# Optimization experiments

Hardware: AMD Instinct MI355X
Metric: run time of the kernel (lower is better)

Reference implementation:

```python
import jax, jax.numpy as jnp
import numpy as np

B, S, DIM = 2, 2048, 4096
NH, NKV, HD = 32, 8, 128
REP = NH // NKV
ROPE_THETA = 10000.0


def _rope(x, cos, sin):
    # x: (B, S, H, HD); cos/sin: (S, HD//2). Interleaved complex rotation.
    xr, xi = x[..., 0::2], x[..., 1::2]
    c = cos[None, :, None, :]
    s = sin[None, :, None, :]
    out_r = xr * c - xi * s
    out_i = xr * s + xi * c
    return jnp.stack([out_r, out_i], axis=-1).reshape(x.shape)


def setup_inputs() -> dict:
    key = jax.random.key(0)
    k0, k1, k2, k3, k4 = jax.random.split(key, 5)
    x = jax.random.normal(k0, (B, S, DIM), jnp.float32)
    std = 0.02
    wq = jax.random.normal(k1, (NH * HD, DIM), jnp.float32) * std
    wk = jax.random.normal(k2, (NKV * HD, DIM), jnp.float32) * std
    wv = jax.random.normal(k3, (NKV * HD, DIM), jnp.float32) * std
    wo = jax.random.normal(k4, (DIM, NH * HD), jnp.float32) * std
    inv_freq = 1.0 / (ROPE_THETA ** (jnp.arange(0, HD, 2, dtype=jnp.float32) / HD))
    ang = jnp.outer(jnp.arange(S, dtype=jnp.float32), inv_freq)  # (S, HD//2)
    return {
        "x": x, "wq": wq, "wk": wk, "wv": wv, "wo": wo,
        "freqs_cos": jnp.cos(ang), "freqs_sin": jnp.sin(ang),
        "start_pos": 0,
    }


def reference(x, wq, wk, wv, wo, freqs_cos, freqs_sin, start_pos):
    bsz, seqlen, _ = x.shape
    q = (x @ wq.T).reshape(bsz, seqlen, NH, HD)
    k = (x @ wk.T).reshape(bsz, seqlen, NKV, HD)
    v = (x @ wv.T).reshape(bsz, seqlen, NKV, HD)
    q = _rope(q, freqs_cos, freqs_sin)
    k = _rope(k, freqs_cos, freqs_sin)
    # Grouped-query attention without materializing repeated KV:
    # q -> (B, NKV, REP, S, HD); k, v -> (B, NKV, S, HD)
    q = q.transpose(0, 2, 1, 3).reshape(bsz, NKV, REP, seqlen, HD)
    k = k.transpose(0, 2, 1, 3)
    v = v.transpose(0, 2, 1, 3)
    scale = 1.0 / jnp.sqrt(jnp.float32(HD))
    scores = jnp.einsum('bgrtd,bgsd->bgrts', q, k) * scale
    causal = jnp.tril(jnp.ones((seqlen, seqlen), dtype=bool))
    scores = jnp.where(causal[None, None, None], scores, jnp.finfo(scores.dtype).min)
    probs = jax.nn.softmax(scores, axis=-1)
    out = jnp.einsum('bgrts,bgsd->bgrtd', probs, v)  # (B, NKV, REP, S, HD)
    out = out.reshape(bsz, NH, seqlen, HD).transpose(0, 2, 1, 3).reshape(bsz, seqlen, NH * HD)
    return out @ wo.T
```

## Files before the change

### kernel.cpp

```cpp
#include <hip/hip_runtime.h>
#include <math.h>

#define B_    2
#define S_    2048
#define DIM_  4096
#define NH_   32
#define NKV_  8
#define HD_   128
#define MROWS (B_ * S_)
#define QDIM  (NH_ * HD_)
#define KVDIM (NKV_ * HD_)

typedef unsigned short ushort_t;
typedef __attribute__((ext_vector_type(8))) short bf16x8;
typedef __attribute__((ext_vector_type(4))) float f32x4;

#define MFMA16(a, b, c) __builtin_amdgcn_mfma_f32_16x16x32_bf16(a, b, c, 0, 0, 0)

__device__ __forceinline__ float bf2f(ushort_t u) {
  return __uint_as_float(((unsigned int)u) << 16);
}
__device__ __forceinline__ ushort_t f2bf(float f) {
  unsigned int x = __float_as_uint(f);
  return (ushort_t)((x + 0x7fffu + ((x >> 16) & 1u)) >> 16);
}
__device__ __forceinline__ void gload16(const void* g, void* l) {
  __builtin_amdgcn_global_load_lds(
      (const __attribute__((address_space(1))) void*)g,
      (__attribute__((address_space(3))) void*)l, 16, 0, 0);
}

__global__ void conv_f32_bf16(const float* __restrict__ in,
                              ushort_t* __restrict__ out) {
  int i = blockIdx.x * 256 + threadIdx.x;
  float4 a = ((const float4*)in)[i * 2 + 0];
  float4 b = ((const float4*)in)[i * 2 + 1];
  bf16x8 o;
  o[0] = (short)f2bf(a.x); o[1] = (short)f2bf(a.y);
  o[2] = (short)f2bf(a.z); o[3] = (short)f2bf(a.w);
  o[4] = (short)f2bf(b.x); o[5] = (short)f2bf(b.y);
  o[6] = (short)f2bf(b.z); o[7] = (short)f2bf(b.w);
  ((bf16x8*)out)[i] = o;
}

template <int OUT_MODE>
__global__ __launch_bounds__(256, 2) void gemm_bf16(
    const ushort_t* __restrict__ A, const ushort_t* __restrict__ W,
    void* __restrict__ Cv, int M, int N, int K) {
  constexpr int BK = 32;
  __shared__ ushort_t As[128 * BK];
  __shared__ ushort_t Ws[128 * BK];
  const int tid = threadIdx.x, lane = tid & 63, w = tid >> 6;
  const int quad = lane >> 4, l16 = lane & 15;
  const int row0 = blockIdx.y * 128, col0 = blockIdx.x * 128;
  const int wm = (w & 1) * 64, wn = (w >> 1) * 64;

  f32x4 acc[4][4] = {};

  for (int k0 = 0; k0 < K; k0 += BK) {
    __syncthreads();
#pragma unroll
    for (int i = 0; i < 2; ++i) {
      int c = i * 256 + w * 64 + lane;
      int r = c >> 2, ko = (c & 3) * 8;
      gload16(A + (size_t)(row0 + r) * K + k0 + ko,
              (char*)As + (i * 256 + w * 64) * 16);
      gload16(W + (size_t)(col0 + r) * K + k0 + ko,
              (char*)Ws + (i * 256 + w * 64) * 16);
    }
    __syncthreads();

    bf16x8 af[4], bfr[4];
#pragma unroll
    for (int mt = 0; mt < 4; ++mt)
      af[mt] = *(const bf16x8*)((char*)As + (wm + mt * 16 + l16) * 64 + quad * 16);
#pragma unroll
    for (int nt = 0; nt < 4; ++nt)
      bfr[nt] = *(const bf16x8*)((char*)Ws + (wn + nt * 16 + l16) * 64 + quad * 16);
#pragma unroll
    for (int mt = 0; mt < 4; ++mt)
#pragma unroll
      for (int nt = 0; nt < 4; ++nt)
        acc[mt][nt] = MFMA16(af[mt], bfr[nt], acc[mt][nt]);
  }

#pragma unroll
  for (int mt = 0; mt < 4; ++mt)
#pragma unroll
    for (int nt = 0; nt < 4; ++nt)
#pragma unroll
      for (int r = 0; r < 4; ++r) {
        int row = row0 + wm + mt * 16 + quad * 4 + r;
        int col = col0 + wn + nt * 16 + l16;
        float v = acc[mt][nt][r];
        if (OUT_MODE == 0)
          ((ushort_t*)Cv)[(size_t)row * N + col] = f2bf(v);
        else if (OUT_MODE == 1)
          ((float*)Cv)[(size_t)row * N + col] = v;
        else
          ((ushort_t*)Cv)[(size_t)col * M + row] = f2bf(v);
      }
}

__global__ void rope_bf16(ushort_t* __restrict__ q, ushort_t* __restrict__ k,
                          const float* __restrict__ cs,
                          const float* __restrict__ sn) {
  int idx = blockIdx.x * 256 + threadIdx.x;
  int jg = (idx & 15) * 4;
  int t = idx >> 4;
  int hh = t % (NH_ + NKV_);
  int bs = t / (NH_ + NKV_);
  int s = bs & (S_ - 1);
  float4 c4 = *(const float4*)(cs + s * 64 + jg);
  float4 s4 = *(const float4*)(sn + s * 64 + jg);
  ushort_t* p = (hh < NH_)
      ? q + (size_t)bs * QDIM + hh * HD_ + 2 * jg
      : k + (size_t)bs * KVDIM + (hh - NH_) * HD_ + 2 * jg;
  bf16x8 v = *(const bf16x8*)p;
  float cc[4] = {c4.x, c4.y, c4.z, c4.w};
  float ss[4] = {s4.x, s4.y, s4.z, s4.w};
  bf16x8 o;
#pragma unroll
  for (int u = 0; u < 4; ++u) {
    float xr = bf2f((ushort_t)v[2 * u]);
    float xi = bf2f((ushort_t)v[2 * u + 1]);
    o[2 * u]     = (short)f2bf(xr * cc[u] - xi * ss[u]);
    o[2 * u + 1] = (short)f2bf(xr * ss[u] + xi * cc[u]);
  }
  *(bf16x8*)p = o;
}

__global__ __launch_bounds__(256, 2) void attn_mfma(
    const ushort_t* __restrict__ qb, const ushort_t* __restrict__ kb,
    const ushort_t* __restrict__ vt, ushort_t* __restrict__ ob) {
  __shared__ __align__(16) char smem[2 * 16384 + 2 * 16384 + 4 * 2304];
  const int tid = threadIdx.x, lane = tid & 63, w = tid >> 6;
  const int quad = lane >> 4, l16 = lane & 15;
  char* psw = smem + 65536 + w * 2304;
  const int h = blockIdx.y, b = blockIdx.z;
  const int kvh = h >> 2;
  const float C = 0.12756113f;

  for (int half = 0; half < 2; ++half) {
    const int qt = (half == 0) ? (S_ / 64 - 1) - blockIdx.x : blockIdx.x;
    const int q0 = qt * 64;

#pragma unroll
    for (int i = 0; i < 4; ++i) {
      int r0 = w * 16 + i * 4;
      int r = r0 + (lane >> 4);
      int c = (lane & 15) ^ (r & 15);
      gload16(qb + (size_t)(b * S_ + q0 + r) * QDIM + h * HD_ + c * 8,
              smem + 16384 + r0 * 256);
      gload16(kb + (size_t)(b * S_ + r) * KVDIM + kvh * HD_ + c * 8,
              smem + r0 * 256);
      int vr0 = w * 32 + i * 8;
      int vr = vr0 + (lane >> 3);
      int vc = (lane & 7) ^ (vr & 7);
      gload16(vt + (size_t)(kvh * HD_ + vr) * MROWS + b * S_ + vc * 8,
              smem + 32768 + vr0 * 128);
    }
    __syncthreads();

    bf16x8 qf[4];
#pragma unroll
    for (int t = 0; t < 4; ++t)
      qf[t] = *(const bf16x8*)(smem + 16384 + (w * 16 + l16) * 256 +
                               (((t * 4 + quad) ^ l16) * 16));
    asm volatile("s_waitcnt lgkmcnt(0)" ::: "memory");

    float m_[4], l_[4];
    f32x4 o_[8] = {};
#pragma unroll
    for (int r = 0; r < 4; ++r) { m_[r] = -1e30f; l_[r] = 0.f; }

    for (int kt = 0; kt <= qt; ++kt) {
      char* Kc = smem + (kt & 1) * 16384;
      char* Vc = smem + 32768 + (kt & 1) * 16384;

      if (kt < qt) {
        char* Kn = smem + ((kt + 1) & 1) * 16384;
        char* Vn = smem + 32768 + ((kt + 1) & 1) * 16384;
#pragma unroll
        for (int i = 0; i < 4; ++i) {
          int r0 = w * 16 + i * 4;
          int r = r0 + (lane >> 4);
          int c = (lane & 15) ^ (r & 15);
          gload16(kb + (size_t)(b * S_ + (kt + 1) * 64 + r) * KVDIM + kvh * HD_ + c * 8,
                  Kn + r0 * 256);
          int vr0 = w * 32 + i * 8;
          int vr = vr0 + (lane >> 3);
          int vc = (lane & 7) ^ (vr & 7);
          gload16(vt + (size_t)(kvh * HD_ + vr) * MROWS + b * S_ + (kt + 1) * 64 + vc * 8,
                  Vn + vr0 * 128);
        }
      }

      const int ntmax = (kt == qt) ? w : 3;
      f32x4 s[4];
      __builtin_amdgcn_s_setprio(1);
#pragma unroll
      for (int nt = 0; nt < 4; ++nt) {
        if (nt <= ntmax) {
          f32x4 a = {0.f, 0.f, 0.f, 0.f};
#pragma unroll
          for (int t = 0; t < 4; ++t) {
            bf16x8 kf = *(const bf16x8*)(Kc + (nt * 16 + l16) * 256 +
                                         (((t * 4 + quad) ^ l16) * 16));
            a = MFMA16(qf[t], kf, a);
          }
          s[nt] = a;
        } else {
          s[nt] = (f32x4){-INFINITY, -INFINITY, -INFINITY, -INFINITY};
        }
      }
      __builtin_amdgcn_s_setprio(0);

      float p[4][4], al[4];
#pragma unroll
      for (int r = 0; r < 4; ++r) {
        float v[4];
#pragma unroll
        for (int nt = 0; nt < 4; ++nt) {
          float vv = s[nt][r] * C;
          if (kt == qt && nt == w && l16 > quad * 4 + r) vv = -INFINITY;
          v[nt] = vv;
        }
        float mx = fmaxf(fmaxf(v[0], v[1]), fmaxf(v[2], v[3]));
#pragma unroll
        for (int d = 1; d < 16; d <<= 1) mx = fmaxf(mx, __shfl_xor(mx, d, 64));
        float mnew = fmaxf(m_[r], mx);
        float a0 = __builtin_amdgcn_exp2f(m_[r] - mnew);
        float sum = 0.f;
#pragma unroll
        for (int nt = 0; nt < 4; ++nt) {
          p[nt][r] = __builtin_amdgcn_exp2f(v[nt] - mnew);
          sum += p[nt][r];
        }
#pragma unroll
        for (int d = 1; d < 16; d <<= 1) sum += __shfl_xor(sum, d, 64);
        l_[r] = l_[r] * a0 + sum;
        m_[r] = mnew;
        al[r] = a0;
      }

#pragma unroll
      for (int r = 0; r < 4; ++r)
#pragma unroll
        for (int nt = 0; nt < 4; ++nt)
          ((ushort_t*)psw)[(quad * 4 + r) * 72 + nt * 16 + l16] = f2bf(p[nt][r]);

#pragma unroll
      for (int dt = 0; dt < 8; ++dt)
#pragma unroll
        for (int r = 0; r < 4; ++r) o_[dt][r] *= al[r];

      asm volatile("s_waitcnt lgkmcnt(0)" ::: "memory");
      bf16x8 pf[2];
#pragma unroll
      for (int kc = 0; kc < 2; ++kc)
        pf[kc] = *(const bf16x8*)(psw + l16 * 144 + kc * 64 + quad * 16);

      __builtin_amdgcn_s_setprio(1);
#pragma unroll
      for (int dt = 0; dt < 8; ++dt) {
#pragma unroll
        for (int kc = 0; kc < 2; ++kc) {
          bf16x8 vf = *(const bf16x8*)(Vc + (dt * 16 + l16) * 128 +
                                       (((kc * 4 + quad) ^ (l16 & 7)) * 16));
          o_[dt] = MFMA16(pf[kc], vf, o_[dt]);
        }
      }
      __builtin_amdgcn_s_setprio(0);

      __syncthreads();
    }

#pragma unroll
    for (int r = 0; r < 4; ++r) {
      float linv = 1.0f / l_[r];
      size_t base = (size_t)(b * S_ + q0 + w * 16 + quad * 4 + r) * QDIM + h * HD_;
#pragma unroll
      for (int dt = 0; dt < 8; ++dt)
        ob[base + dt * 16 + l16] = f2bf(o_[dt][r] * linv);
    }
  }
}

extern "C" void kernel_launch(void* const* d_in, const int* in_sizes, int n_in,
                              void* d_out, int out_size, void* d_ws, size_t ws_size,
                              hipStream_t stream) {
  const float* x  = (const float*)d_in[0];
  const float* wq = (const float*)d_in[1];
  const float* wk = (const float*)d_in[2];
  const float* wv = (const float*)d_in[3];
  const float* wo = (const float*)d_in[4];
  const float* fc = (const float*)d_in[5];
  const float* fs = (const float*)d_in[6];
  float* out = (float*)d_out;

  char* ws = (char*)d_ws;
  ushort_t* xb    = (ushort_t*)(ws);
  ushort_t* wqb   = (ushort_t*)(ws + (32ull << 20));
  ushort_t* wkb   = (ushort_t*)(ws + (64ull << 20));
  ushort_t* wvb   = (ushort_t*)(ws + (72ull << 20));
  ushort_t* qbuf  = (ushort_t*)(ws + (80ull << 20));
  ushort_t* kbuf  = (ushort_t*)(ws + (112ull << 20));
  ushort_t* vtb   = (ushort_t*)(ws + (120ull << 20));
  ushort_t* attnb = (ushort_t*)(ws + (128ull << 20));
  ushort_t* wob   = xb;

  dim3 blk(256);

  conv_f32_bf16<<<(MROWS * DIM_) / 2048, blk, 0, stream>>>(x, xb);
  conv_f32_bf16<<<(QDIM * DIM_) / 2048, blk, 0, stream>>>(wq, wqb);
  conv_f32_bf16<<<(KVDIM * DIM_) / 2048, blk, 0, stream>>>(wk, wkb);
  conv_f32_bf16<<<(KVDIM * DIM_) / 2048, blk, 0, stream>>>(wv, wvb);

  gemm_bf16<0><<<dim3(QDIM / 128, MROWS / 128), blk, 0, stream>>>(xb, wqb, qbuf, MROWS, QDIM, DIM_);
  gemm_bf16<0><<<dim3(KVDIM / 128, MROWS / 128), blk, 0, stream>>>(xb, wkb, kbuf, MROWS, KVDIM, DIM_);
  gemm_bf16<2><<<dim3(KVDIM / 128, MROWS / 128), blk, 0, stream>>>(xb, wvb, vtb, MROWS, KVDIM, DIM_);

  rope_bf16<<<(MROWS * (NH_ + NKV_) * 16) / 256, blk, 0, stream>>>(qbuf, kbuf, fc, fs);

  attn_mfma<<<dim3(S_ / 128, NH_, B_), blk, 0, stream>>>(qbuf, kbuf, vtb, attnb);

  conv_f32_bf16<<<(QDIM * DIM_) / 2048, blk, 0, stream>>>(wo, wob);
  gemm_bf16<1><<<dim3(QDIM / 128, MROWS / 128), blk, 0, stream>>>(attnb, wob, out, MROWS, QDIM, DIM_);
}
```

Baseline: 853.4 us.

## Add 256x256 double-buffered LDS GEMM kernel for Q and output projections

Adds a new 512-thread GEMM kernel that computes a 256x256 output tile per block. It uses XOR-swizzled LDS staging with double buffering, so the next K-slab is loaded while MFMAs run on the current one, and it raises wave priority around the MFMA bursts. The two largest projections, Q and the output projection, now use this kernel instead of the 128x128 one. The aim is more operand reuse per byte loaded and better overlap of global loads with compute. The cost is 128KB of LDS and many accumulator registers per block, which limits occupancy to roughly one block per CU.

Result: faster. 787.3 us (-7.7%).

```diff
diff --git a/kernel.cpp b/kernel.cpp
--- a/kernel.cpp
+++ b/kernel.cpp
@@ -99,6 +99,111 @@
           ((float*)Cv)[(size_t)row * N + col] = v;
         else
           ((ushort_t*)Cv)[(size_t)col * M + row] = f2bf(v);
+      }
+}
+
+__device__ __forceinline__ void stage_half(const ushort_t* __restrict__ src,
+                                           int rowBase, int k0, char* ldsHalf,
+                                           int wid, int lane, int K) {
+#pragma unroll
+  for (int j = 0; j < 2; ++j) {
+    int ct = wid * 64 + j * 512 + lane;
+    int r = ct >> 3, c = ct & 7;
+    gload16(src + (size_t)(rowBase + r) * K + k0 + ((c ^ (r & 7)) << 3),
+            ldsHalf + (wid * 64 + j * 512) * 16);
+  }
+}
+
+__device__ __forceinline__ bf16x8 readfrag(const char* base, int row, int cc) {
+  return *(const bf16x8*)(base + row * 128 + ((cc ^ (row & 7)) << 4));
+}
+
+template <int OUT_MODE>
+__global__ __launch_bounds__(512, 2) void gemm256(
+    const ushort_t* __restrict__ A, const ushort_t* __restrict__ W,
+    void* __restrict__ Cv, int M, int N, int K) {
+  __shared__ __align__(16) char lds[131072];
+  const int tid = threadIdx.x, lane = tid & 63, wid = tid >> 6;
+  const int quad = lane >> 4, l16 = lane & 15;
+  const int wr = wid >> 2, wc = wid & 3;
+  const int row0 = blockIdx.y * 256, col0 = blockIdx.x * 256;
+  const int KT = K >> 6;
+
+  f32x4 acc[8][4] = {};
+
+  stage_half(A, row0,       0, lds,                 wid, lane, K);
+  stage_half(A, row0 + 128, 0, lds + 16384,         wid, lane, K);
+  stage_half(W, col0,       0, lds + 65536,         wid, lane, K);
+  stage_half(W, col0 + 128, 0, lds + 65536 + 16384, wid, lane, K);
+  asm volatile("s_waitcnt vmcnt(0)" ::: "memory");
+  __builtin_amdgcn_s_barrier();
+
+  for (int u = 0; u < KT; ++u) {
+    char* bA = lds + (u & 1) * 32768;
+    char* bB = lds + 65536 + (u & 1) * 32768;
+    char* nA = lds + ((u + 1) & 1) * 32768;
+    char* nB = lds + 65536 + ((u + 1) & 1) * 32768;
+    const bool st = (u + 1 < KT);
+    const int kn = (u + 1) << 6;
+
+    bf16x8 bfrag[4][2];
+#pragma unroll
+    for (int ph = 0; ph < 4; ++ph) {
+      bf16x8 afr[2][2];
+#pragma unroll
+      for (int mi = 0; mi < 2; ++mi)
+#pragma unroll
+        for (int kc = 0; kc < 2; ++kc)
+          afr[mi][kc] =
+              readfrag(bA, wr * 128 + (ph * 2 + mi) * 16 + l16, kc * 4 + quad);
+      if (ph == 0) {
+#pragma unroll
+        for (int nt = 0; nt < 4; ++nt)
+#pragma unroll
+          for (int kc = 0; kc < 2; ++kc)
+            bfrag[nt][kc] = readfrag(bB, wc * 64 + nt * 16 + l16, kc * 4 + quad);
+        if (st) {
+          stage_half(A, row0,       kn, nA,         wid, lane, K);
+          stage_half(A, row0 + 128, kn, nA + 16384, wid, lane, K);
+        }
+      }
+      if (ph == 1 && st) {
+        stage_half(W, col0,       kn, nB,         wid, lane, K);
+        stage_half(W, col0 + 128, kn, nB + 16384, wid, lane, K);
+      }
+
+      __builtin_amdgcn_s_barrier();
+      asm volatile("s_waitcnt lgkmcnt(0)" ::: "memory");
+      __builtin_amdgcn_sched_barrier(0);
+      __builtin_amdgcn_s_setprio(1);
+#pragma unroll
+      for (int mi = 0; mi < 2; ++mi)
+#pragma unroll
+        for (int nt = 0; nt < 4; ++nt)
+#pragma unroll
+          for (int kc = 0; kc < 2; ++kc)
+            acc[ph * 2 + mi][nt] =
+                MFMA16(afr[mi][kc], bfrag[nt][kc], acc[ph * 2 + mi][nt]);
+      __builtin_amdgcn_s_setprio(0);
+      if (ph == 3)
+        asm volatile("s_waitcnt vmcnt(0)" ::: "memory");
+      __builtin_amdgcn_s_barrier();
+    }
+  }
+
+#pragma unroll
+  for (int mt = 0; mt < 8; ++mt)
+#pragma unroll
+    for (int nt = 0; nt < 4; ++nt)
+#pragma unroll
+      for (int r = 0; r < 4; ++r) {
+        int row = row0 + wr * 128 + mt * 16 + quad * 4 + r;
+        int col = col0 + wc * 64 + nt * 16 + l16;
+        float v = acc[mt][nt][r];
+        if (OUT_MODE == 0)
+          ((ushort_t*)Cv)[(size_t)row * N + col] = f2bf(v);
+        else
+          ((float*)Cv)[(size_t)row * N + col] = v;
       }
 }
 
@@ -311,13 +416,14 @@
   ushort_t* wob   = xb;
 
   dim3 blk(256);
+  dim3 blk512(512);
 
   conv_f32_bf16<<<(MROWS * DIM_) / 2048, blk, 0, stream>>>(x, xb);
   conv_f32_bf16<<<(QDIM * DIM_) / 2048, blk, 0, stream>>>(wq, wqb);
   conv_f32_bf16<<<(KVDIM * DIM_) / 2048, blk, 0, stream>>>(wk, wkb);
   conv_f32_bf16<<<(KVDIM * DIM_) / 2048, blk, 0, stream>>>(wv, wvb);
 
-  gemm_bf16<0><<<dim3(QDIM / 128, MROWS / 128), blk, 0, stream>>>(xb, wqb, qbuf, MROWS, QDIM, DIM_);
+  gemm256<0><<<dim3(QDIM / 256, MROWS / 256), blk512, 0, stream>>>(xb, wqb, qbuf, MROWS, QDIM, DIM_);
   gemm_bf16<0><<<dim3(KVDIM / 128, MROWS / 128), blk, 0, stream>>>(xb, wkb, kbuf, MROWS, KVDIM, DIM_);
   gemm_bf16<2><<<dim3(KVDIM / 128, MROWS / 128), blk, 0, stream>>>(xb, wvb, vtb, MROWS, KVDIM, DIM_);
 
@@ -326,5 +432,5 @@
   attn_mfma<<<dim3(S_ / 128, NH_, B_), blk, 0, stream>>>(qbuf, kbuf, vtb, attnb);
 
   conv_f32_bf16<<<(QDIM * DIM_) / 2048, blk, 0, stream>>>(wo, wob);
-  gemm_bf16<1><<<dim3(QDIM / 128, MROWS / 128), blk, 0, stream>>>(attnb, wob, out, MROWS, QDIM, DIM_);
-}
+  gemm256<1><<<dim3(QDIM / 256, MROWS / 256), blk512, 0, stream>>>(attnb, wob, out, MROWS, QDIM, DIM_);
+}
```
